# Kernel optimization log

Measured on AMD Instinct MI355X. Metric: run time of the kernel, lower is better.

Reference implementation:

```python
import math
import jax, jax.numpy as jnp
import numpy as np

B, S, H, NH, BS, R = 2, 4096, 1024, 16, 64, 3
HD = H // NH          # 64 head dim
L = S // BS           # 64 blocks
PEN = -10000.0


def _make_rand_attn():
    # data-independent random block plan (like HF bigbird, seeded numpy),
    # per head, per middle query block: R random key blocks excluding
    # global blocks (0, L-1) and the sliding window (i-1, i, i+1)
    rng = np.random.RandomState(42)
    ra = np.zeros((NH, L - 2, R), dtype=np.int64)
    for h in range(NH):
        for i in range(1, L - 1):
            choices = np.array([j for j in range(L) if j not in (0, i - 1, i, i + 1, L - 1)])
            ra[h, i - 1] = rng.choice(choices, R, replace=False)
    return ra


def setup_inputs():
    key = jax.random.key(0)
    ks = jax.random.split(key, 8)
    sc = 1.0 / math.sqrt(H)
    return {
        "Q": jax.random.normal(ks[0], (B, S, H), jnp.float32),
        "K": jax.random.normal(ks[1], (B, S, H), jnp.float32),
        "V": jax.random.normal(ks[2], (B, S, H), jnp.float32),
        "mask": jnp.ones((B, S), jnp.float32),
        "Wq": jax.random.normal(ks[3], (H, H), jnp.float32) * sc,
        "bq": jnp.zeros((H,), jnp.float32),
        "Wk": jax.random.normal(ks[4], (H, H), jnp.float32) * sc,
        "bk": jnp.zeros((H,), jnp.float32),
        "Wv": jax.random.normal(ks[5], (H, H), jnp.float32) * sc,
        "bv": jnp.zeros((H,), jnp.float32),
        "rand_attn": jnp.asarray(_make_rand_attn()),
    }


def _forward(Q, K, V, mask, Wq, bq, Wk, bk, Wv, bv, rand_attn):
    rsd = 1.0 / math.sqrt(HD)
    sm = lambda x: jax.nn.softmax(x, axis=-1)

    def proj(x, W, b):  # torch Linear: x @ W^T + b, then split heads
        return (x @ W.T + b).reshape(B, S, NH, HD).transpose(0, 2, 1, 3)

    q = proj(Q, Wq, bq)  # [B,NH,S,HD]
    k = proj(K, Wk, bk)
    v = proj(V, Wv, bv)
    qb = q.reshape(B, NH, L, BS, HD)
    kb = k.reshape(B, NH, L, BS, HD)
    vb = v.reshape(B, NH, L, BS, HD)

    # ---- masks (derived from padding mask, as in HF create_masks_...) ----
    blocked = mask.reshape(B, L, BS)
    from_mask = mask[:, None, :, None]   # [B,1,S,1]
    to_mask = mask[:, None, None, :]     # [B,1,1,S]
    exp_to = jnp.concatenate([blocked[:, 1:-3], blocked[:, 2:-2], blocked[:, 3:-1]], axis=2)  # [B,L-4,3BS]
    band_mask = jnp.einsum('blq,blk->blqk', blocked[:, 2:-2], exp_to)[:, None]  # [B,1,L-4,BS,3BS]

    ra = jnp.broadcast_to(rand_attn[None], (B, NH, L - 2, R))
    bidx = jnp.arange(B)[:, None, None, None]
    hidx = jnp.arange(NH)[None, :, None, None]
    gk = kb[bidx, hidx, ra].reshape(B, NH, L - 2, R * BS, HD)  # gathered random key blocks
    gv = vb[bidx, hidx, ra].reshape(B, NH, L - 2, R * BS, HD)
    rm = blocked[bidx, ra].reshape(B, NH, L - 2, R * BS)
    rand_mask = jnp.einsum('blq,bhlk->bhlqk', blocked[:, 1:-1], rm)  # [B,NH,L-2,BS,R*BS]

    # ---- first block: dense attention over all keys ----
    p1 = jnp.einsum('bhqd,bhkd->bhqk', qb[:, :, 0], k) * rsd + (1.0 - to_mask) * PEN
    ctx_first = jnp.einsum('bhqk,bhkd->bhqd', sm(p1), v)

    # ---- second block: global(0) + window(1,2) + last + random ----
    k2 = jnp.concatenate([kb[:, :, 0], kb[:, :, 1], kb[:, :, 2], kb[:, :, -1], gk[:, :, 0]], axis=2)
    v2 = jnp.concatenate([vb[:, :, 0], vb[:, :, 1], vb[:, :, 2], vb[:, :, -1], gv[:, :, 0]], axis=2)
    p2 = jnp.einsum('bhqd,bhkd->bhqk', qb[:, :, 1], k2) * rsd
    seq_pad2 = jnp.concatenate([to_mask[..., :3 * BS], to_mask[..., -BS:],
                                jnp.ones((B, 1, 1, R * BS), mask.dtype)], axis=3)
    rand_pad2 = jnp.concatenate([jnp.ones((B, NH, BS, 4 * BS), mask.dtype), rand_mask[:, :, 0]], axis=3)
    p2 = p2 + (1.0 - jnp.minimum(seq_pad2, rand_pad2)) * PEN
    ctx_second = jnp.einsum('bhqk,bhkd->bhqd', sm(p2), v2)

    # ---- middle blocks: band (3 sliding) + random + 2 global ----
    exp_k = jnp.concatenate([kb[:, :, 1:-3], kb[:, :, 2:-2], kb[:, :, 3:-1]], axis=3)  # [B,NH,L-4,3BS,HD]
    exp_v = jnp.concatenate([vb[:, :, 1:-3], vb[:, :, 2:-2], vb[:, :, 3:-1]], axis=3)
    mq = qb[:, :, 2:-2]
    inner = jnp.einsum('bhlqd,bhlkd->bhlqk', mq, exp_k) * rsd + (1.0 - band_mask) * PEN
    randp = jnp.einsum('bhlqd,bhlkd->bhlqk', mq, gk[:, :, 1:-1]) * rsd + (1.0 - rand_mask[:, :, 1:-1]) * PEN
    firstp = jnp.einsum('bhlqd,bhkd->bhlqk', mq, kb[:, :, 0]) * rsd + (1.0 - to_mask[:, :, :, None, :BS]) * PEN
    lastp = jnp.einsum('bhlqd,bhkd->bhlqk', mq, kb[:, :, -1]) * rsd + (1.0 - to_mask[:, :, :, None, -BS:]) * PEN
    w = sm(jnp.concatenate([firstp, inner, randp, lastp], axis=-1))  # [B,NH,L-4,BS,(5+R)*BS]
    ctx_mid = jnp.einsum('bhlqk,bhlkd->bhlqd', w[..., BS:4 * BS], exp_v)
    ctx_mid += jnp.einsum('bhlqk,bhlkd->bhlqd', w[..., 4 * BS:(4 + R) * BS], gv[:, :, 1:-1])
    ctx_mid += jnp.einsum('bhlqk,bhkd->bhlqd', w[..., :BS], vb[:, :, 0])
    ctx_mid += jnp.einsum('bhlqk,bhkd->bhlqd', w[..., -BS:], vb[:, :, -1])

    # ---- second-to-last block ----
    k3 = jnp.concatenate([kb[:, :, 0], kb[:, :, -3], kb[:, :, -2], kb[:, :, -1], gk[:, :, -1]], axis=2)
    v3 = jnp.concatenate([vb[:, :, 0], vb[:, :, -3], vb[:, :, -2], vb[:, :, -1], gv[:, :, -1]], axis=2)
    p3 = jnp.einsum('bhqd,bhkd->bhqk', qb[:, :, -2], k3) * rsd
    seq_pad3 = jnp.concatenate([to_mask[..., :BS], to_mask[..., -3 * BS:],
                                jnp.ones((B, 1, 1, R * BS), mask.dtype)], axis=3)
    rand_pad3 = jnp.concatenate([jnp.ones((B, NH, BS, 4 * BS), mask.dtype), rand_mask[:, :, -1]], axis=3)
    p3 = p3 + (1.0 - jnp.minimum(seq_pad3, rand_pad3)) * PEN
    ctx_seclast = jnp.einsum('bhqk,bhkd->bhqd', sm(p3), v3)

    # ---- last block: dense attention over all keys ----
    p4 = jnp.einsum('bhqd,bhkd->bhqk', qb[:, :, -1], k) * rsd + (1.0 - to_mask) * PEN
    ctx_last = jnp.einsum('bhqk,bhkd->bhqd', sm(p4), v)

    ctx = jnp.concatenate([ctx_first[:, :, None], ctx_second[:, :, None], ctx_mid,
                           ctx_seclast[:, :, None], ctx_last[:, :, None]], axis=2)
    ctx = ctx.reshape(B, NH, S, HD) * from_mask
    return ctx.transpose(0, 2, 1, 3).reshape(B, S, NH * HD)


def reference(Q, K, V, mask, Wq, bq, Wk, bk, Wv, bv, rand_attn):
    return _forward(Q, K, V, mask, Wq, bq, Wk, bk, Wv, bv, rand_attn)
```

## Files before the change

kernel.cpp:

```cpp
#include <hip/hip_runtime.h>
#include <hip/hip_bf16.h>
#include <stdint.h>

#define BB 2
#define SS 4096
#define HH 1024
#define NHh 16
#define HD 64
#define LL 64
#define BS 64
#define RR 3
#define PENf (-10000.0f)

typedef unsigned int uint;
typedef __attribute__((ext_vector_type(8))) short bf16x8;
typedef __attribute__((ext_vector_type(4))) float f32x4;

__device__ __forceinline__ ushort f2bf(float f) {
    union { float f; uint u; } v; v.f = f;
    uint u = v.u;
    return (ushort)((u + 0x7fffu + ((u >> 16) & 1u)) >> 16);
}
__device__ __forceinline__ uint pack_bf(float a, float b) {
    uint r;
    asm("v_cvt_pk_bf16_f32 %0, %1, %2" : "=v"(r) : "v"(a), "v"(b));
    return r;
}
__device__ __forceinline__ uint scale_pair(uint w) {
    float lo = __uint_as_float(w << 16) * 0.125f;
    float hi = __uint_as_float(w & 0xffff0000u) * 0.125f;
    return pack_bf(lo, hi);
}
__device__ __forceinline__ uint4 scale4(uint4 w) {
    uint4 o;
    o.x = scale_pair(w.x); o.y = scale_pair(w.y);
    o.z = scale_pair(w.z); o.w = scale_pair(w.w);
    return o;
}
__device__ __forceinline__ void async16(const ushort* g, ushort* l) {
    __builtin_amdgcn_global_load_lds((const __attribute__((address_space(1))) uint*)g,
                                     (__attribute__((address_space(3))) uint*)l,
                                     16, 0, 0);
}

__global__ __launch_bounds__(256)
void cvt_kernel(const float* __restrict__ Xq, const float* __restrict__ Xk,
                const float* __restrict__ Xv, const float* __restrict__ Wq,
                const float* __restrict__ Wk, const float* __restrict__ Wv,
                ushort* __restrict__ Xbf, ushort* __restrict__ Wbf)
{
    const size_t XTOT = (size_t)3 * BB * SS * HH;
    const uint u = blockIdx.x * 256 + threadIdx.x;
    const size_t e = (size_t)u * 8;
    const float* src; ushort* dst;
    if (e < XTOT) {
        const int zz = (int)(e >> 23);
        src = (zz == 0 ? Xq : zz == 1 ? Xk : Xv) + (e & ((1u << 23) - 1));
        dst = Xbf + e;
    } else {
        const size_t e2 = e - XTOT;
        const int zz = (int)(e2 >> 20);
        src = (zz == 0 ? Wq : zz == 1 ? Wk : Wv) + (e2 & ((1u << 20) - 1));
        dst = Wbf + e2;
    }
    float4 a = ((const float4*)src)[0];
    float4 c = ((const float4*)src)[1];
    uint4 o;
    o.x = pack_bf(a.x, a.y); o.y = pack_bf(a.z, a.w);
    o.z = pack_bf(c.x, c.y); o.w = pack_bf(c.z, c.w);
    *(uint4*)dst = o;
}

__global__ __launch_bounds__(256)
void gemm3_kernel(const ushort* __restrict__ Xbf, const ushort* __restrict__ Wbf,
                  const float* __restrict__ bq, const float* __restrict__ bk,
                  const float* __restrict__ bv,
                  ushort* __restrict__ qb, ushort* __restrict__ kb,
                  ushort* __restrict__ vbT)
{
    __shared__ __align__(16) ushort smem[128 * 136];
    ushort* As = smem;
    ushort* Bs = smem + 8192;

    const int z = blockIdx.z;
    const ushort* A  = Xbf + (size_t)z * ((size_t)BB * SS * HH);
    const ushort* Bt = Wbf + (size_t)z * (HH * HH);
    const float* bias = (z == 0) ? bq : (z == 1) ? bk : bv;

    const int tid = threadIdx.x;
    const int m0 = blockIdx.x * 128;
    const int n0 = blockIdx.y * 128;
    const int wave = tid >> 6;
    const int lane = tid & 63;
    const int l15 = lane & 15;
    const int quad = lane >> 4;
    const int wr = wave >> 1, wc = wave & 1;

    f32x4 acc[4][4];
#pragma unroll
    for (int i = 0; i < 4; ++i)
#pragma unroll
        for (int j = 0; j < 4; ++j) acc[i][j] = (f32x4){0.f, 0.f, 0.f, 0.f};

    const int p8 = (lane & 3) * 8;
    const ushort* Abase = A + (size_t)(m0 + wave * 32 + (lane >> 2)) * HH + p8;
    const ushort* Bbase = Bt + (size_t)(n0 + wave * 32 + (lane >> 2)) * HH + p8;

#define STAGE_G(k0, bp)                                        \
    do {                                                       \
        ushort* A0 = As + (bp) * 4096 + wave * 1024;           \
        ushort* B0 = Bs + (bp) * 4096 + wave * 1024;           \
        async16(Abase + (k0), A0);                             \
        async16(Abase + 16 * HH + (k0), A0 + 512);             \
        async16(Bbase + (k0), B0);                             \
        async16(Bbase + 16 * HH + (k0), B0 + 512);             \
    } while (0)

    STAGE_G(0, 0);
    for (int k0 = 0, bp = 0; k0 < HH; k0 += 32, bp ^= 1) {
        __syncthreads();
        if (k0 + 32 < HH) STAGE_G(k0 + 32, bp ^ 1);
        bf16x8 af[4], bfr[4];
#pragma unroll
        for (int mt = 0; mt < 4; ++mt)
            af[mt] = *(const bf16x8*)(As + bp * 4096 + (wr * 64 + mt * 16 + l15) * 32 + quad * 8);
#pragma unroll
        for (int nt = 0; nt < 4; ++nt)
            bfr[nt] = *(const bf16x8*)(Bs + bp * 4096 + (wc * 64 + nt * 16 + l15) * 32 + quad * 8);
        if (z < 2) {
#pragma unroll
            for (int i = 0; i < 4; ++i)
#pragma unroll
                for (int j = 0; j < 4; ++j)
                    acc[i][j] = __builtin_amdgcn_mfma_f32_16x16x32_bf16(bfr[i], af[j], acc[i][j], 0, 0, 0);
        } else {
#pragma unroll
            for (int i = 0; i < 4; ++i)
#pragma unroll
                for (int j = 0; j < 4; ++j)
                    acc[i][j] = __builtin_amdgcn_mfma_f32_16x16x32_bf16(af[i], bfr[j], acc[i][j], 0, 0, 0);
        }
    }
#undef STAGE_G

    if (z < 2) {
        ushort* outp = (z == 0) ? qb : kb;
#pragma unroll
        for (int wt = 0; wt < 4; ++wt) {
            const int n_base = n0 + wc * 64 + wt * 16 + quad * 4;
            const float4 b4 = *(const float4*)&bias[n_base];
            const int nh = n_base >> 6;
            const int hd = n_base & 63;
#pragma unroll
            for (int xt = 0; xt < 4; ++xt) {
                const int m = m0 + wr * 64 + xt * 16 + l15;
                const int bgl = m >> 12, s = m & 4095;
                uint2 pk;
                pk.x = pack_bf(acc[wt][xt][0] + b4.x, acc[wt][xt][1] + b4.y);
                pk.y = pack_bf(acc[wt][xt][2] + b4.z, acc[wt][xt][3] + b4.w);
                *(uint2*)&outp[((size_t)((bgl << 4) | nh) * SS + s) * HD + hd] = pk;
            }
        }
    } else {
        __syncthreads();
        ushort* stg = smem;
#pragma unroll
        for (int nt = 0; nt < 4; ++nt) {
            const int n_local = wc * 64 + nt * 16 + l15;
            const float bn = bias[n0 + n_local];
#pragma unroll
            for (int mt = 0; mt < 4; ++mt) {
                const int m_base = wr * 64 + mt * 16 + quad * 4;
                uint2 pk;
                pk.x = pack_bf(acc[mt][nt][0] + bn, acc[mt][nt][1] + bn);
                pk.y = pack_bf(acc[mt][nt][2] + bn, acc[mt][nt][3] + bn);
                *(uint2*)(stg + n_local * 136 + m_base) = pk;
            }
        }
        __syncthreads();
        const int n_row = tid >> 1;
        const int half = tid & 1;
        const int n = n0 + n_row;
        const int nh = n >> 6, hd = n & 63;
        const int bgl = m0 >> 12;
        const int sbase = (m0 & 4095) + half * 64;
        const uint4* src = (const uint4*)(stg + n_row * 136 + half * 64);
        uint4* dst = (uint4*)(vbT + ((size_t)((bgl << 4) | nh) * HD + hd) * SS + sbase);
#pragma unroll
        for (int j = 0; j < 8; ++j) dst[j] = src[j];
    }
}

__global__ __launch_bounds__(256)
void proj3_kernel(const float* __restrict__ Xq, const float* __restrict__ Xk,
                  const float* __restrict__ Xv,
                  const float* __restrict__ Wq, const float* __restrict__ Wk,
                  const float* __restrict__ Wv,
                  const float* __restrict__ bq, const float* __restrict__ bk,
                  const float* __restrict__ bv,
                  ushort* __restrict__ qb, ushort* __restrict__ kb,
                  ushort* __restrict__ vbT)
{
    __shared__ __align__(16) ushort smem[128 * 136];
    ushort* As = smem;
    ushort* Bs = smem + 128 * 40;

    const int z = blockIdx.z;
    const float* X    = (z == 0) ? Xq : (z == 1) ? Xk : Xv;
    const float* W    = (z == 0) ? Wq : (z == 1) ? Wk : Wv;
    const float* bias = (z == 0) ? bq : (z == 1) ? bk : bv;

    const int tid = threadIdx.x;
    const int m0 = blockIdx.x * 128;
    const int n0 = blockIdx.y * 128;
    const int wave = tid >> 6;
    const int lane = tid & 63;
    const int l15 = lane & 15;
    const int quad = lane >> 4;
    const int wr = wave >> 1, wc = wave & 1;

    f32x4 acc[4][4];
#pragma unroll
    for (int mt = 0; mt < 4; ++mt)
#pragma unroll
        for (int nt = 0; nt < 4; ++nt) acc[mt][nt] = (f32x4){0.f, 0.f, 0.f, 0.f};

    const int srow = tid >> 1;
    const int shalf = tid & 1;
    const float* xp = X + (size_t)(m0 + srow) * HH + shalf * 16;
    const float* wp = W + (size_t)(n0 + srow) * HH + shalf * 16;
    ushort* asw = As + srow * 40 + shalf * 16;
    ushort* bsw = Bs + srow * 40 + shalf * 16;

    for (int k0 = 0; k0 < HH; k0 += 32) {
        float4 a0 = *(const float4*)(xp + k0);
        float4 a1 = *(const float4*)(xp + k0 + 4);
        float4 a2 = *(const float4*)(xp + k0 + 8);
        float4 a3 = *(const float4*)(xp + k0 + 12);
        float4 b0 = *(const float4*)(wp + k0);
        float4 b1 = *(const float4*)(wp + k0 + 4);
        float4 b2 = *(const float4*)(wp + k0 + 8);
        float4 b3 = *(const float4*)(wp + k0 + 12);
        __syncthreads();
        uint4 pa, pb;
        pa.x = pack_bf(a0.x, a0.y); pa.y = pack_bf(a0.z, a0.w);
        pa.z = pack_bf(a1.x, a1.y); pa.w = pack_bf(a1.z, a1.w);
        *(uint4*)asw = pa;
        pa.x = pack_bf(a2.x, a2.y); pa.y = pack_bf(a2.z, a2.w);
        pa.z = pack_bf(a3.x, a3.y); pa.w = pack_bf(a3.z, a3.w);
        *(uint4*)(asw + 8) = pa;
        pb.x = pack_bf(b0.x, b0.y); pb.y = pack_bf(b0.z, b0.w);
        pb.z = pack_bf(b1.x, b1.y); pb.w = pack_bf(b1.z, b1.w);
        *(uint4*)bsw = pb;
        pb.x = pack_bf(b2.x, b2.y); pb.y = pack_bf(b2.z, b2.w);
        pb.z = pack_bf(b3.x, b3.y); pb.w = pack_bf(b3.z, b3.w);
        *(uint4*)(bsw + 8) = pb;
        __syncthreads();

        bf16x8 af[4], bfr[4];
#pragma unroll
        for (int mt = 0; mt < 4; ++mt)
            af[mt] = *(const bf16x8*)(As + (wr * 64 + mt * 16 + l15) * 40 + quad * 8);
#pragma unroll
        for (int nt = 0; nt < 4; ++nt)
            bfr[nt] = *(const bf16x8*)(Bs + (wc * 64 + nt * 16 + l15) * 40 + quad * 8);
#pragma unroll
        for (int mt = 0; mt < 4; ++mt)
#pragma unroll
            for (int nt = 0; nt < 4; ++nt)
                acc[mt][nt] = __builtin_amdgcn_mfma_f32_16x16x32_bf16(af[mt], bfr[nt], acc[mt][nt], 0, 0, 0);
    }

    if (z < 2) {
        ushort* outp = (z == 0) ? qb : kb;
#pragma unroll
        for (int nt = 0; nt < 4; ++nt) {
            const int n = n0 + wc * 64 + nt * 16 + l15;
            const float bn = bias[n];
            const int nh = n >> 6, hd = n & 63;
#pragma unroll
            for (int mt = 0; mt < 4; ++mt) {
#pragma unroll
                for (int rr = 0; rr < 4; ++rr) {
                    const int m = m0 + wr * 64 + mt * 16 + quad * 4 + rr;
                    const int bgl = m >> 12, s = m & 4095;
                    outp[((size_t)((bgl << 4) | nh) * SS + s) * HD + hd] = f2bf(acc[mt][nt][rr] + bn);
                }
            }
        }
    } else {
        __syncthreads();
        ushort* stg = smem;
#pragma unroll
        for (int nt = 0; nt < 4; ++nt) {
            const int n_local = wc * 64 + nt * 16 + l15;
            const float bn = bias[n0 + n_local];
#pragma unroll
            for (int mt = 0; mt < 4; ++mt) {
                const int m_base = wr * 64 + mt * 16 + quad * 4;
                uint2 pk;
                pk.x = pack_bf(acc[mt][nt][0] + bn, acc[mt][nt][1] + bn);
                pk.y = pack_bf(acc[mt][nt][2] + bn, acc[mt][nt][3] + bn);
                *(uint2*)(stg + n_local * 136 + m_base) = pk;
            }
        }
        __syncthreads();
        const int n_row = tid >> 1;
        const int half = tid & 1;
        const int n = n0 + n_row;
        const int nh = n >> 6, hd = n & 63;
        const int bgl = m0 >> 12;
        const int sbase = (m0 & 4095) + half * 64;
        const uint4* src = (const uint4*)(stg + n_row * 136 + half * 64);
        uint4* dst = (uint4*)(vbT + ((size_t)((bgl << 4) | nh) * HD + hd) * SS + sbase);
#pragma unroll
        for (int j = 0; j < 8; ++j) dst[j] = src[j];
    }
}

__global__ __launch_bounds__(256)
void attn_kernel(const ushort* __restrict__ qg, const ushort* __restrict__ kg,
                 const ushort* __restrict__ vTg,
                 const float* __restrict__ mask, const int* __restrict__ rand_attn,
                 float* __restrict__ out, float* __restrict__ partO,
                 float* __restrict__ partML)
{
    __shared__ __align__(16) ushort qs_ps[64][72];
    __shared__ __align__(16) ushort ks2[2][2][64][32];
    __shared__ __align__(16) ushort vs2[2][2][64][32];
    __shared__ __align__(16) float qm_s[64];
    __shared__ __align__(16) float km_s[2][64];

    const int tid = threadIdx.x;
    const int wid = blockIdx.x;
    const int bh = wid / 78;
    const int r = wid - bh * 78;
    const int b = bh >> 4, h = bh & 15;

    int i, nkb;
    int kbl[8], pfl[8];
    bool dense;
    int part = 0, which = 0;
    if (r < 62) {
        dense = false;
        i = r + 1;
        const int* ra = rand_attn + ((size_t)h * (LL - 2) + (i - 1)) * RR;
        if (i == 1) {
            kbl[0] = 0; kbl[1] = 1; kbl[2] = 2; kbl[3] = LL - 1;
            kbl[4] = ra[0]; kbl[5] = ra[1]; kbl[6] = ra[2]; kbl[7] = 0;
            pfl[0] = pfl[1] = pfl[2] = pfl[3] = 0;
            pfl[4] = pfl[5] = pfl[6] = 1; pfl[7] = 0;
            nkb = 7;
        } else if (i == LL - 2) {
            kbl[0] = 0; kbl[1] = LL - 3; kbl[2] = LL - 2; kbl[3] = LL - 1;
            kbl[4] = ra[0]; kbl[5] = ra[1]; kbl[6] = ra[2]; kbl[7] = 0;
            pfl[0] = pfl[1] = pfl[2] = pfl[3] = 0;
            pfl[4] = pfl[5] = pfl[6] = 1; pfl[7] = 0;
            nkb = 7;
        } else {
            kbl[0] = 0;      pfl[0] = 0;
            kbl[1] = i - 1;  pfl[1] = 1;
            kbl[2] = i;      pfl[2] = 1;
            kbl[3] = i + 1;  pfl[3] = 1;
            kbl[4] = LL - 1; pfl[4] = 0;
            kbl[5] = ra[0]; kbl[6] = ra[1]; kbl[7] = ra[2];
            pfl[5] = pfl[6] = pfl[7] = 1;
            nkb = 8;
        }
    } else {
        dense = true;
        const int r2 = r - 62;
        which = r2 >> 3;
        part = r2 & 7;
        i = which ? (LL - 1) : 0;
        nkb = 8;
#pragma unroll
        for (int j = 0; j < 8; ++j) { kbl[j] = part * 8 + j; pfl[j] = 0; }
    }

    const int lane = tid & 63;
    const int wave = tid >> 6;
    const int l15 = lane & 15;
    const int quad = lane >> 4;
    const int srow = lane >> 2;
    const int p8s = (((lane & 3) ^ ((srow >> 1) & 3))) * 8;
    const ushort* kgb = kg + (size_t)bh * SS * HD;
    const ushort* vgb = vTg + (size_t)bh * HD * SS;

#define STAGE_KV(kb_, bp)                                                        \
    do {                                                                         \
        const size_t krow = (size_t)((kb_) * BS + wave * 16 + srow) * HD;        \
        async16(kgb + krow + p8s,      &ks2[bp][0][wave * 16][0]);               \
        async16(kgb + krow + 32 + p8s, &ks2[bp][1][wave * 16][0]);               \
        const size_t vrow = (size_t)(wave * 16 + srow) * SS + (kb_) * BS;        \
        async16(vgb + vrow + p8s,      &vs2[bp][0][wave * 16][0]);               \
        async16(vgb + vrow + 32 + p8s, &vs2[bp][1][wave * 16][0]);               \
    } while (0)

    {
        const int row = tid >> 2;
        const int c0 = (tid & 3) * 16;
        const ushort* src = qg + ((size_t)bh * SS + i * BS + row) * HD + c0;
        uint4 w0 = *(const uint4*)src;
        uint4 w1 = *(const uint4*)(src + 8);
        *(uint4*)&qs_ps[row][c0] = scale4(w0);
        *(uint4*)&qs_ps[row][c0 + 8] = scale4(w1);
        if (tid < 64) qm_s[tid] = mask[(size_t)b * SS + i * BS + tid];
    }
    STAGE_KV(kbl[0], 0);
    if (tid < 64) km_s[0][tid] = mask[(size_t)b * SS + kbl[0] * BS + tid];
    __syncthreads();

    bf16x8 aq[2];
    aq[0] = *(const bf16x8*)&qs_ps[wave * 16 + l15][quad * 8];
    aq[1] = *(const bf16x8*)&qs_ps[wave * 16 + l15][32 + quad * 8];
    const float qm = qm_s[wave * 16 + l15];

    const int sqz = (quad ^ ((l15 >> 1) & 3)) * 8;

    float mrow = -1e30f, lrow = 0.0f;
    f32x4 accO[4];
#pragma unroll
    for (int dt = 0; dt < 4; ++dt) accO[dt] = (f32x4){0.f, 0.f, 0.f, 0.f};

    for (int it = 0; it < nkb; ++it) {
        const int cur = it & 1;
        if (it + 1 < nkb) {
            STAGE_KV(kbl[it + 1], cur ^ 1);
            if (tid < 64) km_s[cur ^ 1][tid] = mask[(size_t)b * SS + kbl[it + 1] * BS + tid];
        }
        const int pf = pfl[it];

        f32x4 sc[4];
#pragma unroll
        for (int nt = 0; nt < 4; ++nt) sc[nt] = (f32x4){0.f, 0.f, 0.f, 0.f};
#pragma unroll
        for (int c = 0; c < 2; ++c) {
#pragma unroll
            for (int nt = 0; nt < 4; ++nt) {
                bf16x8 af = *(const bf16x8*)&ks2[cur][c][nt * 16 + l15][sqz];
                sc[nt] = __builtin_amdgcn_mfma_f32_16x16x32_bf16(af, aq[c], sc[nt], 0, 0, 0);
            }
        }

        float p[4][4];
        float bm = -1e30f;
#pragma unroll
        for (int nt = 0; nt < 4; ++nt) {
            const float4 km4 = *(const float4*)&km_s[cur][nt * 16 + quad * 4];
            const float kmv[4] = {km4.x, km4.y, km4.z, km4.w};
#pragma unroll
            for (int rr = 0; rr < 4; ++rr) {
                const float pm = pf ? (qm * kmv[rr]) : kmv[rr];
                const float sv = sc[nt][rr] + (1.0f - pm) * PENf;
                p[nt][rr] = sv;
                bm = fmaxf(bm, sv);
            }
        }
        bm = fmaxf(bm, __shfl_xor(bm, 16));
        bm = fmaxf(bm, __shfl_xor(bm, 32));
        if (!__all(bm - mrow <= 8.0f)) {
            const float mn = fmaxf(mrow, bm);
            const float alpha = __expf(mrow - mn);
            mrow = mn;
            float a4[4];
#pragma unroll
            for (int rr = 0; rr < 4; ++rr) a4[rr] = __shfl(alpha, quad * 4 + rr, 64);
#pragma unroll
            for (int dt = 0; dt < 4; ++dt) {
#pragma unroll
                for (int rr = 0; rr < 4; ++rr) accO[dt][rr] *= a4[rr];
            }
            lrow *= alpha;
        }
        float ls = 0.0f;
#pragma unroll
        for (int nt = 0; nt < 4; ++nt)
#pragma unroll
            for (int rr = 0; rr < 4; ++rr) {
                p[nt][rr] = __expf(p[nt][rr] - mrow);
                ls += p[nt][rr];
            }
        ls += __shfl_xor(ls, 16);
        ls += __shfl_xor(ls, 32);
        lrow += ls;

#pragma unroll
        for (int nt = 0; nt < 4; ++nt) {
            uint2 pk;
            pk.x = pack_bf(p[nt][0], p[nt][1]);
            pk.y = pack_bf(p[nt][2], p[nt][3]);
            *(uint2*)&qs_ps[wave * 16 + l15][nt * 16 + quad * 4] = pk;
        }

#pragma unroll
        for (int c = 0; c < 2; ++c) {
            bf16x8 ap = *(const bf16x8*)&qs_ps[wave * 16 + l15][c * 32 + quad * 8];
#pragma unroll
            for (int dt = 0; dt < 4; ++dt) {
                bf16x8 bvf = *(const bf16x8*)&vs2[cur][c][dt * 16 + l15][sqz];
                accO[dt] = __builtin_amdgcn_mfma_f32_16x16x32_bf16(ap, bvf, accO[dt], 0, 0, 0);
            }
        }

        if (it + 1 < nkb) __syncthreads();
    }
#undef STAGE_KV

    if (!dense) {
#pragma unroll
        for (int rr = 0; rr < 4; ++rr) {
            const int qloc = quad * 4 + rr;
            const float lq = __shfl(lrow, qloc, 64);
            const float inv = qm_s[wave * 16 + qloc] / lq;
#pragma unroll
            for (int dt = 0; dt < 4; ++dt) {
                const int d = dt * 16 + l15;
                out[((size_t)b * SS + i * BS + wave * 16 + qloc) * HH + h * HD + d] = accO[dt][rr] * inv;
            }
        }
    } else {
        const int slot = (bh * 2 + which) * 8 + part;
        float* po = partO + (size_t)slot * 4096;
#pragma unroll
        for (int rr = 0; rr < 4; ++rr) {
            const int qrow = wave * 16 + quad * 4 + rr;
#pragma unroll
            for (int dt = 0; dt < 4; ++dt) {
                const int d = dt * 16 + l15;
                po[qrow * 64 + d] = accO[dt][rr];
            }
        }
        if (lane < 16) {
            partML[slot * 128 + wave * 16 + lane] = mrow;
            partML[slot * 128 + 64 + wave * 16 + lane] = lrow;
        }
    }
}

__global__ __launch_bounds__(64)
void combine_kernel(const float* __restrict__ partO, const float* __restrict__ partML,
                    const float* __restrict__ mask, float* __restrict__ out)
{
    const int g4 = blockIdx.x;
    const int g = g4 >> 2;
    const int bh = g >> 1, which = g & 1;
    const int b = bh >> 4, h = bh & 15;
    const int i = which ? (LL - 1) : 0;
    const int t = threadIdx.x;
    const int row = ((g4 & 3) << 4) | (t >> 2);
    const int d0 = (t & 3) * 16;
    const int base = g * 8;

    float mp[8], lp[8];
    float M = -1e30f;
#pragma unroll
    for (int p = 0; p < 8; ++p) {
        mp[p] = partML[(base + p) * 128 + row];
        lp[p] = partML[(base + p) * 128 + 64 + row];
        M = fmaxf(M, mp[p]);
    }
    float L = 0.0f, w[8];
#pragma unroll
    for (int p = 0; p < 8; ++p) { w[p] = __expf(mp[p] - M); L += lp[p] * w[p]; }

    float4 o[4];
#pragma unroll
    for (int j = 0; j < 4; ++j) o[j] = make_float4(0.f, 0.f, 0.f, 0.f);
#pragma unroll
    for (int p = 0; p < 8; ++p) {
        const float* po = partO + (size_t)(base + p) * 4096 + row * 64 + d0;
#pragma unroll
        for (int j = 0; j < 4; ++j) {
            float4 v = *(const float4*)(po + j * 4);
            o[j].x = fmaf(w[p], v.x, o[j].x);
            o[j].y = fmaf(w[p], v.y, o[j].y);
            o[j].z = fmaf(w[p], v.z, o[j].z);
            o[j].w = fmaf(w[p], v.w, o[j].w);
        }
    }
    const float fm = mask[(size_t)b * SS + i * BS + row];
    const float inv = fm / L;
    float* dst = out + ((size_t)b * SS + i * BS + row) * HH + h * HD + d0;
#pragma unroll
    for (int j = 0; j < 4; ++j) {
        float4 v;
        v.x = o[j].x * inv; v.y = o[j].y * inv;
        v.z = o[j].z * inv; v.w = o[j].w * inv;
        *(float4*)(dst + j * 4) = v;
    }
}

extern "C" void kernel_launch(void* const* d_in, const int* in_sizes, int n_in,
                              void* d_out, int out_size, void* d_ws, size_t ws_size,
                              hipStream_t stream) {
    (void)in_sizes; (void)n_in; (void)out_size;
    const float* Q    = (const float*)d_in[0];
    const float* K    = (const float*)d_in[1];
    const float* V    = (const float*)d_in[2];
    const float* mask = (const float*)d_in[3];
    const float* Wq   = (const float*)d_in[4];
    const float* bq   = (const float*)d_in[5];
    const float* Wk   = (const float*)d_in[6];
    const float* bk   = (const float*)d_in[7];
    const float* Wv   = (const float*)d_in[8];
    const float* bv   = (const float*)d_in[9];
    const int*   ra   = (const int*)d_in[10];
    float* out = (float*)d_out;

    const size_t qkv = (size_t)BB * NHh * SS * HD;
    ushort* qb  = (ushort*)d_ws;
    ushort* kb  = qb + qkv;
    ushort* vbT = kb + qkv;
    float* partO  = (float*)(vbT + qkv);
    float* partML = partO + (size_t)512 * 4096;
    ushort* Xbf = (ushort*)(partML + (size_t)512 * 128);
    ushort* Wbf = Xbf + 3 * qkv;
    const size_t need = (size_t)((char*)(Wbf + (size_t)3 * HH * HH) - (char*)d_ws);

    if (ws_size >= need) {
        cvt_kernel<<<13824, 256, 0, stream>>>(Q, K, V, Wq, Wk, Wv, Xbf, Wbf);
        gemm3_kernel<<<dim3(64, 8, 3), 256, 0, stream>>>(Xbf, Wbf, bq, bk, bv, qb, kb, vbT);
    } else {
        proj3_kernel<<<dim3(64, 8, 3), 256, 0, stream>>>(Q, K, V, Wq, Wk, Wv, bq, bk, bv,
                                                         qb, kb, vbT);
    }
    attn_kernel<<<dim3(BB * NHh * 78), 256, 0, stream>>>(qb, kb, vbT, mask, ra,
                                                         out, partO, partML);
    combine_kernel<<<dim3(BB * NHh * 2 * 4), 64, 0, stream>>>(partO, partML, mask, out);
}
```

Baseline: 292.3 us.

## Enlarge QKV projection GEMM to 256x256 tiles with 4-stage async pipeline

```diff
diff --git a/kernel.cpp b/kernel.cpp
--- a/kernel.cpp
+++ b/kernel.cpp
@@ -71,123 +71,158 @@
     *(uint4*)dst = o;
 }
 
-__global__ __launch_bounds__(256)
-void gemm3_kernel(const ushort* __restrict__ Xbf, const ushort* __restrict__ Wbf,
+__global__ __launch_bounds__(512, 2)
+void gemm8_kernel(const ushort* __restrict__ Xbf, const ushort* __restrict__ Wbf,
                   const float* __restrict__ bq, const float* __restrict__ bk,
                   const float* __restrict__ bv,
                   ushort* __restrict__ qb, ushort* __restrict__ kb,
                   ushort* __restrict__ vbT)
 {
-    __shared__ __align__(16) ushort smem[128 * 136];
-    ushort* As = smem;
-    ushort* Bs = smem + 8192;
+    __shared__ __align__(16) ushort smem8[65536];
+    ushort* As_ = smem8;
+    ushort* Bs_ = smem8 + 32768;
 
     const int z = blockIdx.z;
-    const ushort* A  = Xbf + (size_t)z * ((size_t)BB * SS * HH);
-    const ushort* Bt = Wbf + (size_t)z * (HH * HH);
+    const ushort* Ag = Xbf + (size_t)z * ((size_t)BB * SS * HH);
+    const ushort* Bg = Wbf + (size_t)z * (HH * HH);
     const float* bias = (z == 0) ? bq : (z == 1) ? bk : bv;
+    const bool zv = (z == 2);
 
     const int tid = threadIdx.x;
-    const int m0 = blockIdx.x * 128;
-    const int n0 = blockIdx.y * 128;
+    const int m0 = blockIdx.x * 256;
+    const int n0 = blockIdx.y * 256;
     const int wave = tid >> 6;
     const int lane = tid & 63;
     const int l15 = lane & 15;
     const int quad = lane >> 4;
-    const int wr = wave >> 1, wc = wave & 1;
-
-    f32x4 acc[4][4];
-#pragma unroll
-    for (int i = 0; i < 4; ++i)
-#pragma unroll
-        for (int j = 0; j < 4; ++j) acc[i][j] = (f32x4){0.f, 0.f, 0.f, 0.f};
-
-    const int p8 = (lane & 3) * 8;
-    const ushort* Abase = A + (size_t)(m0 + wave * 32 + (lane >> 2)) * HH + p8;
-    const ushort* Bbase = Bt + (size_t)(n0 + wave * 32 + (lane >> 2)) * HH + p8;
-
-#define STAGE_G(k0, bp)                                        \
-    do {                                                       \
-        ushort* A0 = As + (bp) * 4096 + wave * 1024;           \
-        ushort* B0 = Bs + (bp) * 4096 + wave * 1024;           \
-        async16(Abase + (k0), A0);                             \
-        async16(Abase + 16 * HH + (k0), A0 + 512);             \
-        async16(Bbase + (k0), B0);                             \
-        async16(Bbase + 16 * HH + (k0), B0 + 512);             \
+    const int wr = wave >> 2;
+    const int wc = wave & 3;
+
+    f32x4 acc[8][4];
+#pragma unroll
+    for (int mi = 0; mi < 8; ++mi)
+#pragma unroll
+        for (int ni = 0; ni < 4; ++ni) acc[mi][ni] = (f32x4){0.f, 0.f, 0.f, 0.f};
+
+    const int trow = tid >> 2;
+    const int tcol = ((tid & 3) ^ ((tid >> 3) & 3)) * 8;
+    const ushort* Ath = Ag + (size_t)(m0 + trow) * HH + tcol;
+    const ushort* Bth = Bg + (size_t)(n0 + trow) * HH + tcol;
+    const int sl8 = (quad ^ ((l15 >> 1) & 3)) * 8;
+
+#define STAGE8(kt_)                                                   \
+    do {                                                              \
+        const int k0_ = (kt_) * 32;                                   \
+        const int sb_ = ((kt_) & 3) * 8192 + wave * 512;              \
+        async16(Ath + k0_,            As_ + sb_);                     \
+        async16(Ath + 128 * HH + k0_, As_ + sb_ + 4096);              \
+        async16(Bth + k0_,            Bs_ + sb_);                     \
+        async16(Bth + 128 * HH + k0_, Bs_ + sb_ + 4096);              \
     } while (0)
 
-    STAGE_G(0, 0);
-    for (int k0 = 0, bp = 0; k0 < HH; k0 += 32, bp ^= 1) {
-        __syncthreads();
-        if (k0 + 32 < HH) STAGE_G(k0 + 32, bp ^ 1);
-        bf16x8 af[4], bfr[4];
-#pragma unroll
-        for (int mt = 0; mt < 4; ++mt)
-            af[mt] = *(const bf16x8*)(As + bp * 4096 + (wr * 64 + mt * 16 + l15) * 32 + quad * 8);
-#pragma unroll
-        for (int nt = 0; nt < 4; ++nt)
-            bfr[nt] = *(const bf16x8*)(Bs + bp * 4096 + (wc * 64 + nt * 16 + l15) * 32 + quad * 8);
-        if (z < 2) {
-#pragma unroll
-            for (int i = 0; i < 4; ++i)
-#pragma unroll
-                for (int j = 0; j < 4; ++j)
-                    acc[i][j] = __builtin_amdgcn_mfma_f32_16x16x32_bf16(bfr[i], af[j], acc[i][j], 0, 0, 0);
-        } else {
-#pragma unroll
-            for (int i = 0; i < 4; ++i)
-#pragma unroll
-                for (int j = 0; j < 4; ++j)
-                    acc[i][j] = __builtin_amdgcn_mfma_f32_16x16x32_bf16(af[i], bfr[j], acc[i][j], 0, 0, 0);
-        }
-    }
-#undef STAGE_G
-
-    if (z < 2) {
+#define TILE_BODY(kt_, VM_, DOSTAGE_)                                              \
+    do {                                                                           \
+        const int bp_ = (kt_) & 3;                                                 \
+        asm volatile("s_waitcnt vmcnt(" #VM_ ")" ::: "memory");                    \
+        __builtin_amdgcn_s_barrier();                                              \
+        __builtin_amdgcn_sched_barrier(0);                                         \
+        const ushort* Ab_ = As_ + bp_ * 8192;                                      \
+        const ushort* Bb_ = Bs_ + bp_ * 8192;                                      \
+        bf16x8 af_[8], bf_[4];                                                     \
+        _Pragma("unroll")                                                          \
+        for (int ni = 0; ni < 4; ++ni)                                             \
+            bf_[ni] = *(const bf16x8*)(Bb_ + (wc * 64 + ni * 16 + l15) * 32 + sl8);\
+        _Pragma("unroll")                                                          \
+        for (int mi = 0; mi < 8; ++mi)                                             \
+            af_[mi] = *(const bf16x8*)(Ab_ + (wr * 128 + mi * 16 + l15) * 32 + sl8);\
+        if (DOSTAGE_) STAGE8((kt_) + 3);                                           \
+        __builtin_amdgcn_s_setprio(1);                                             \
+        if (zv) {                                                                  \
+            _Pragma("unroll")                                                      \
+            for (int mi = 0; mi < 8; ++mi)                                         \
+                _Pragma("unroll")                                                  \
+                for (int ni = 0; ni < 4; ++ni)                                     \
+                    acc[mi][ni] = __builtin_amdgcn_mfma_f32_16x16x32_bf16(         \
+                        af_[mi], bf_[ni], acc[mi][ni], 0, 0, 0);                   \
+        } else {                                                                   \
+            _Pragma("unroll")                                                      \
+            for (int mi = 0; mi < 8; ++mi)                                         \
+                _Pragma("unroll")                                                  \
+                for (int ni = 0; ni < 4; ++ni)                                     \
+                    acc[mi][ni] = __builtin_amdgcn_mfma_f32_16x16x32_bf16(         \
+                        bf_[ni], af_[mi], acc[mi][ni], 0, 0, 0);                   \
+        }                                                                          \
+        __builtin_amdgcn_s_setprio(0);                                             \
+    } while (0)
+
+    STAGE8(0); STAGE8(1); STAGE8(2);
+
+    for (int k4 = 0; k4 < 28; k4 += 4) {
+        TILE_BODY(k4 + 0, 8, 1);
+        TILE_BODY(k4 + 1, 8, 1);
+        TILE_BODY(k4 + 2, 8, 1);
+        TILE_BODY(k4 + 3, 8, 1);
+    }
+    TILE_BODY(28, 8, 1);
+    TILE_BODY(29, 8, 0);
+    TILE_BODY(30, 4, 0);
+    TILE_BODY(31, 0, 0);
+#undef TILE_BODY
+#undef STAGE8
+
+    if (!zv) {
         ushort* outp = (z == 0) ? qb : kb;
 #pragma unroll
-        for (int wt = 0; wt < 4; ++wt) {
-            const int n_base = n0 + wc * 64 + wt * 16 + quad * 4;
-            const float4 b4 = *(const float4*)&bias[n_base];
-            const int nh = n_base >> 6;
-            const int hd = n_base & 63;
-#pragma unroll
-            for (int xt = 0; xt < 4; ++xt) {
-                const int m = m0 + wr * 64 + xt * 16 + l15;
+        for (int ni = 0; ni < 4; ++ni) {
+            const int nb = n0 + wc * 64 + ni * 16 + quad * 4;
+            const float4 b4 = *(const float4*)&bias[nb];
+            const int nh = nb >> 6;
+            const int hd = nb & 63;
+#pragma unroll
+            for (int mi = 0; mi < 8; ++mi) {
+                const int m = m0 + wr * 128 + mi * 16 + l15;
                 const int bgl = m >> 12, s = m & 4095;
                 uint2 pk;
-                pk.x = pack_bf(acc[wt][xt][0] + b4.x, acc[wt][xt][1] + b4.y);
-                pk.y = pack_bf(acc[wt][xt][2] + b4.z, acc[wt][xt][3] + b4.w);
+                pk.x = pack_bf(acc[mi][ni][0] + b4.x, acc[mi][ni][1] + b4.y);
+                pk.y = pack_bf(acc[mi][ni][2] + b4.z, acc[mi][ni][3] + b4.w);
                 *(uint2*)&outp[((size_t)((bgl << 4) | nh) * SS + s) * HD + hd] = pk;
             }
         }
     } else {
         __syncthreads();
-        ushort* stg = smem;
-#pragma unroll
-        for (int nt = 0; nt < 4; ++nt) {
-            const int n_local = wc * 64 + nt * 16 + l15;
-            const float bn = bias[n0 + n_local];
-#pragma unroll
-            for (int mt = 0; mt < 4; ++mt) {
-                const int m_base = wr * 64 + mt * 16 + quad * 4;
-                uint2 pk;
-                pk.x = pack_bf(acc[mt][nt][0] + bn, acc[mt][nt][1] + bn);
-                pk.y = pack_bf(acc[mt][nt][2] + bn, acc[mt][nt][3] + bn);
-                *(uint2*)(stg + n_local * 136 + m_base) = pk;
-            }
-        }
-        __syncthreads();
-        const int n_row = tid >> 1;
-        const int half = tid & 1;
-        const int n = n0 + n_row;
-        const int nh = n >> 6, hd = n & 63;
+        ushort* stg = smem8;
         const int bgl = m0 >> 12;
-        const int sbase = (m0 & 4095) + half * 64;
-        const uint4* src = (const uint4*)(stg + n_row * 136 + half * 64);
-        uint4* dst = (uint4*)(vbT + ((size_t)((bgl << 4) | nh) * HD + hd) * SS + sbase);
-#pragma unroll
-        for (int j = 0; j < 8; ++j) dst[j] = src[j];
+#pragma unroll
+        for (int p = 0; p < 2; ++p) {
+            __syncthreads();
+            if ((wc >> 1) == p) {
+#pragma unroll
+                for (int ni = 0; ni < 4; ++ni) {
+                    const int nl = (wc & 1) * 64 + ni * 16 + l15;
+                    const float bn = bias[n0 + p * 128 + nl];
+#pragma unroll
+                    for (int mi = 0; mi < 8; ++mi) {
+                        const int mb = wr * 128 + mi * 16 + quad * 4;
+                        uint2 pk;
+                        pk.x = pack_bf(acc[mi][ni][0] + bn, acc[mi][ni][1] + bn);
+                        pk.y = pack_bf(acc[mi][ni][2] + bn, acc[mi][ni][3] + bn);
+                        *(uint2*)(stg + nl * 272 + mb) = pk;
+                    }
+                }
+            }
+            __syncthreads();
+            {
+                const int row = tid >> 2;
+                const int seg = tid & 3;
+                const int n = n0 + p * 128 + row;
+                const int nh = n >> 6, hd = n & 63;
+                const uint4* src = (const uint4*)(stg + row * 272 + seg * 64);
+                uint4* dst = (uint4*)(vbT + ((size_t)((bgl << 4) | nh) * HD + hd) * SS
+                                      + (m0 & 4095) + seg * 64);
+#pragma unroll
+                for (int jj = 0; jj < 8; ++jj) dst[jj] = src[jj];
+            }
+        }
     }
 }
 
@@ -620,7 +655,7 @@
 
     if (ws_size >= need) {
         cvt_kernel<<<13824, 256, 0, stream>>>(Q, K, V, Wq, Wk, Wv, Xbf, Wbf);
-        gemm3_kernel<<<dim3(64, 8, 3), 256, 0, stream>>>(Xbf, Wbf, bq, bk, bv, qb, kb, vbT);
+        gemm8_kernel<<<dim3(32, 4, 3), 512, 0, stream>>>(Xbf, Wbf, bq, bk, bv, qb, kb, vbT);
     } else {
         proj3_kernel<<<dim3(64, 8, 3), 256, 0, stream>>>(Q, K, V, Wq, Wk, Wv, bq, bk, bv,
                                                          qb, kb, vbT);
```

Result: slower. 559.7 us (+91.5%).

## Widen projection GEMM tile to 128x256 with 4-stage async pipeline and swizzled LDS

Applied to the files above, without the earlier changes.

```diff
diff --git a/kernel.cpp b/kernel.cpp
--- a/kernel.cpp
+++ b/kernel.cpp
@@ -71,30 +71,30 @@
     *(uint4*)dst = o;
 }
 
-__global__ __launch_bounds__(256)
-void gemm3_kernel(const ushort* __restrict__ Xbf, const ushort* __restrict__ Wbf,
+__global__ __launch_bounds__(512)
+void gemm6_kernel(const ushort* __restrict__ Xbf, const ushort* __restrict__ Wbf,
                   const float* __restrict__ bq, const float* __restrict__ bk,
                   const float* __restrict__ bv,
                   ushort* __restrict__ qb, ushort* __restrict__ kb,
                   ushort* __restrict__ vbT)
 {
-    __shared__ __align__(16) ushort smem[128 * 136];
-    ushort* As = smem;
-    ushort* Bs = smem + 8192;
+    __shared__ __align__(16) ushort smem6[49152];
 
     const int z = blockIdx.z;
-    const ushort* A  = Xbf + (size_t)z * ((size_t)BB * SS * HH);
-    const ushort* Bt = Wbf + (size_t)z * (HH * HH);
+    const ushort* Ag = Xbf + (size_t)z * ((size_t)BB * SS * HH);
+    const ushort* Bg = Wbf + (size_t)z * (HH * HH);
     const float* bias = (z == 0) ? bq : (z == 1) ? bk : bv;
+    const bool zv = (z == 2);
 
     const int tid = threadIdx.x;
     const int m0 = blockIdx.x * 128;
-    const int n0 = blockIdx.y * 128;
+    const int n0 = blockIdx.y * 256;
     const int wave = tid >> 6;
     const int lane = tid & 63;
     const int l15 = lane & 15;
     const int quad = lane >> 4;
-    const int wr = wave >> 1, wc = wave & 1;
+    const int wr = wave >> 2;
+    const int wc = wave & 3;
 
     f32x4 acc[4][4];
 #pragma unroll
@@ -102,55 +102,80 @@
 #pragma unroll
         for (int j = 0; j < 4; ++j) acc[i][j] = (f32x4){0.f, 0.f, 0.f, 0.f};
 
-    const int p8 = (lane & 3) * 8;
-    const ushort* Abase = A + (size_t)(m0 + wave * 32 + (lane >> 2)) * HH + p8;
-    const ushort* Bbase = Bt + (size_t)(n0 + wave * 32 + (lane >> 2)) * HH + p8;
-
-#define STAGE_G(k0, bp)                                        \
-    do {                                                       \
-        ushort* A0 = As + (bp) * 4096 + wave * 1024;           \
-        ushort* B0 = Bs + (bp) * 4096 + wave * 1024;           \
-        async16(Abase + (k0), A0);                             \
-        async16(Abase + 16 * HH + (k0), A0 + 512);             \
-        async16(Bbase + (k0), B0);                             \
-        async16(Bbase + 16 * HH + (k0), B0 + 512);             \
+    const int trow = tid >> 2;
+    const int tcol = ((tid & 3) ^ ((tid >> 3) & 3)) * 8;
+    const ushort* Ath  = Ag + (size_t)(m0 + trow) * HH + tcol;
+    const ushort* Bth  = Bg + (size_t)(n0 + trow) * HH + tcol;
+    const ushort* Bth2 = Bth + (size_t)128 * HH;
+    const int sl8 = (quad ^ ((l15 >> 1) & 3)) * 8;
+
+#define STAGE6(kt_)                                                    \
+    do {                                                               \
+        const int k0_ = (kt_) * 32;                                    \
+        const int sb_ = ((kt_) & 3) * 12288 + wave * 512;              \
+        async16(Ath + k0_,  smem6 + sb_);                              \
+        async16(Bth + k0_,  smem6 + sb_ + 4096);                       \
+        async16(Bth2 + k0_, smem6 + sb_ + 8192);                       \
     } while (0)
 
-    STAGE_G(0, 0);
-    for (int k0 = 0, bp = 0; k0 < HH; k0 += 32, bp ^= 1) {
-        __syncthreads();
-        if (k0 + 32 < HH) STAGE_G(k0 + 32, bp ^ 1);
-        bf16x8 af[4], bfr[4];
-#pragma unroll
-        for (int mt = 0; mt < 4; ++mt)
-            af[mt] = *(const bf16x8*)(As + bp * 4096 + (wr * 64 + mt * 16 + l15) * 32 + quad * 8);
-#pragma unroll
-        for (int nt = 0; nt < 4; ++nt)
-            bfr[nt] = *(const bf16x8*)(Bs + bp * 4096 + (wc * 64 + nt * 16 + l15) * 32 + quad * 8);
-        if (z < 2) {
-#pragma unroll
-            for (int i = 0; i < 4; ++i)
-#pragma unroll
-                for (int j = 0; j < 4; ++j)
-                    acc[i][j] = __builtin_amdgcn_mfma_f32_16x16x32_bf16(bfr[i], af[j], acc[i][j], 0, 0, 0);
-        } else {
-#pragma unroll
-            for (int i = 0; i < 4; ++i)
-#pragma unroll
-                for (int j = 0; j < 4; ++j)
-                    acc[i][j] = __builtin_amdgcn_mfma_f32_16x16x32_bf16(af[i], bfr[j], acc[i][j], 0, 0, 0);
-        }
-    }
-#undef STAGE_G
-
-    if (z < 2) {
+#define TB6(kt_, VM_, DOSTAGE_)                                                     \
+    do {                                                                            \
+        const int bo_ = ((kt_) & 3) * 12288;                                        \
+        asm volatile("s_waitcnt vmcnt(" #VM_ ")" ::: "memory");                     \
+        __builtin_amdgcn_s_barrier();                                               \
+        __builtin_amdgcn_sched_barrier(0);                                          \
+        const ushort* Ab_ = smem6 + bo_;                                            \
+        const ushort* Bb_ = smem6 + bo_ + 4096;                                     \
+        bf16x8 af_[4], bf_[4];                                                      \
+        _Pragma("unroll")                                                           \
+        for (int mt = 0; mt < 4; ++mt)                                              \
+            af_[mt] = *(const bf16x8*)(Ab_ + (wr * 64 + mt * 16 + l15) * 32 + sl8); \
+        _Pragma("unroll")                                                           \
+        for (int nt = 0; nt < 4; ++nt)                                              \
+            bf_[nt] = *(const bf16x8*)(Bb_ + (wc * 64 + nt * 16 + l15) * 32 + sl8); \
+        if (DOSTAGE_) STAGE6((kt_) + 3);                                            \
+        __builtin_amdgcn_s_setprio(1);                                              \
+        if (zv) {                                                                   \
+            _Pragma("unroll")                                                       \
+            for (int i = 0; i < 4; ++i)                                             \
+                _Pragma("unroll")                                                   \
+                for (int j = 0; j < 4; ++j)                                         \
+                    acc[i][j] = __builtin_amdgcn_mfma_f32_16x16x32_bf16(            \
+                        af_[i], bf_[j], acc[i][j], 0, 0, 0);                        \
+        } else {                                                                    \
+            _Pragma("unroll")                                                       \
+            for (int i = 0; i < 4; ++i)                                             \
+                _Pragma("unroll")                                                   \
+                for (int j = 0; j < 4; ++j)                                         \
+                    acc[i][j] = __builtin_amdgcn_mfma_f32_16x16x32_bf16(            \
+                        bf_[i], af_[j], acc[i][j], 0, 0, 0);                        \
+        }                                                                           \
+        __builtin_amdgcn_s_setprio(0);                                              \
+    } while (0)
+
+    STAGE6(0); STAGE6(1); STAGE6(2);
+
+    for (int k4 = 0; k4 < 28; k4 += 4) {
+        TB6(k4 + 0, 6, 1);
+        TB6(k4 + 1, 6, 1);
+        TB6(k4 + 2, 6, 1);
+        TB6(k4 + 3, 6, 1);
+    }
+    TB6(28, 6, 1);
+    TB6(29, 6, 0);
+    TB6(30, 3, 0);
+    TB6(31, 0, 0);
+#undef TB6
+#undef STAGE6
+
+    if (!zv) {
         ushort* outp = (z == 0) ? qb : kb;
 #pragma unroll
         for (int wt = 0; wt < 4; ++wt) {
-            const int n_base = n0 + wc * 64 + wt * 16 + quad * 4;
-            const float4 b4 = *(const float4*)&bias[n_base];
-            const int nh = n_base >> 6;
-            const int hd = n_base & 63;
+            const int nb = n0 + wc * 64 + wt * 16 + quad * 4;
+            const float4 b4 = *(const float4*)&bias[nb];
+            const int nh = nb >> 6;
+            const int hd = nb & 63;
 #pragma unroll
             for (int xt = 0; xt < 4; ++xt) {
                 const int m = m0 + wr * 64 + xt * 16 + l15;
@@ -163,7 +188,8 @@
         }
     } else {
         __syncthreads();
-        ushort* stg = smem;
+        ushort* stg = smem6;
+        const int bgl = m0 >> 12;
 #pragma unroll
         for (int nt = 0; nt < 4; ++nt) {
             const int n_local = wc * 64 + nt * 16 + l15;
@@ -182,12 +208,11 @@
         const int half = tid & 1;
         const int n = n0 + n_row;
         const int nh = n >> 6, hd = n & 63;
-        const int bgl = m0 >> 12;
-        const int sbase = (m0 & 4095) + half * 64;
         const uint4* src = (const uint4*)(stg + n_row * 136 + half * 64);
-        uint4* dst = (uint4*)(vbT + ((size_t)((bgl << 4) | nh) * HD + hd) * SS + sbase);
-#pragma unroll
-        for (int j = 0; j < 8; ++j) dst[j] = src[j];
+        uint4* dst = (uint4*)(vbT + ((size_t)((bgl << 4) | nh) * HD + hd) * SS
+                              + (m0 & 4095) + half * 64);
+#pragma unroll
+        for (int jj = 0; jj < 8; ++jj) dst[jj] = src[jj];
     }
 }
 
@@ -620,7 +645,7 @@
 
     if (ws_size >= need) {
         cvt_kernel<<<13824, 256, 0, stream>>>(Q, K, V, Wq, Wk, Wv, Xbf, Wbf);
-        gemm3_kernel<<<dim3(64, 8, 3), 256, 0, stream>>>(Xbf, Wbf, bq, bk, bv, qb, kb, vbT);
+        gemm6_kernel<<<dim3(64, 4, 3), 512, 0, stream>>>(Xbf, Wbf, bq, bk, bv, qb, kb, vbT);
     } else {
         proj3_kernel<<<dim3(64, 8, 3), 256, 0, stream>>>(Q, K, V, Wq, Wk, Wv, bq, bk, bv,
                                                          qb, kb, vbT);
```

New measurement: 280.9 us. 1.04x faster.
